# Optimization experiments

Measured on AMD Instinct MI355X. Metric: run time of the kernel, lower is better.

## Reference

```python
import jax, jax.numpy as jnp
import numpy as np

B, IN, H = 16384, 10, 1024
GD_ITERS, GD_LR = 7, 0.001


def setup_inputs() -> dict:
    key = jax.random.key(0)
    ks = jax.random.split(key, 16)
    s_in = 1.0 / np.sqrt(IN)
    s_h = 1.0 / np.sqrt(H)
    inp = {
        'x': jax.random.normal(ks[0], (B, IN), jnp.float32),
        'hidden': jax.random.normal(ks[1], (B, H), jnp.float32),
        'c': jax.random.normal(ks[2], (B, H), jnp.float32),
        'mid_price': jax.random.normal(ks[3], (B,), jnp.float32),
        # nn.Linear weights are [out, in]; biases [out]
        'Wf_w': jax.random.uniform(ks[4], (H, IN), jnp.float32, -s_in, s_in),
        'Wf_b': jax.random.uniform(ks[5], (H,), jnp.float32, -s_in, s_in),
        'Uf_w': jax.random.uniform(ks[6], (H, H), jnp.float32, -s_h, s_h),
        'Wi_w': jax.random.uniform(ks[7], (H, IN), jnp.float32, -s_in, s_in),
        'Wi_b': jax.random.uniform(ks[8], (H,), jnp.float32, -s_in, s_in),
        'Ui_w': jax.random.uniform(ks[9], (H, H), jnp.float32, -s_h, s_h),
        'Wc_w': jax.random.uniform(ks[10], (H, IN), jnp.float32, -s_in, s_in),
        'Wc_b': jax.random.uniform(ks[11], (H,), jnp.float32, -s_in, s_in),
        'Uc_w': jax.random.uniform(ks[12], (H, H), jnp.float32, -s_h, s_h),
        'Wo_w': jax.random.uniform(ks[13], (H, IN), jnp.float32, -s_in, s_in),
        'Wo_b': jax.random.uniform(ks[14], (H,), jnp.float32, -s_in, s_in),
        'Uo_w': jax.random.uniform(ks[15], (H, H), jnp.float32, -s_h, s_h),
    }
    return inp


def reference(x, hidden, c, mid_price, Wf_w, Wf_b, Uf_w, Wi_w, Wi_b, Ui_w,
              Wc_w, Wc_b, Uc_w, Wo_w, Wo_b, Uo_w):
    mp = mid_price.reshape(-1, 1)                       # [B,1]
    f_t = jax.nn.sigmoid(x @ Wf_w.T + Wf_b + hidden @ Uf_w.T)
    i_t = jax.nn.sigmoid(x @ Wi_w.T + Wi_b + hidden @ Ui_w.T)
    c_tilda = jnp.tanh(x @ Wc_w.T + Wc_b + hidden @ Uc_w.T)
    o_t = jax.nn.sigmoid(x @ Wo_w.T + Wo_b + hidden @ Uo_w.T)
    c_new = f_t * c + i_t * c_tilda
    h_std = o_t * jnp.tanh(c_new)
    r_t = jnp.concatenate([f_t, i_t, c_tilda, o_t, c_new, h_std], axis=1)  # [B,6H]

    bsz = r_t.shape[0]
    theta = jnp.zeros((6 * H, 1), dtype=r_t.dtype)

    def gd_step(_, th):
        err = r_t @ th - mp                             # [B,1]
        grad = 2.0 * (r_t.T @ err) / bsz                # [6H,1]
        return th - GD_LR * grad

    theta = jax.lax.fori_loop(0, GD_ITERS, gd_step, theta)

    importance = jnp.mean(jnp.abs(theta.reshape(6, H)), axis=1)  # [6]
    max_idx = jnp.argmax(importance)
    h_new = jax.lax.dynamic_slice(r_t, (0, max_idx * H), (bsz, H))
    return (h_new, c_new)
```

## Files before the change

kernel.cpp:

```cpp
#include <hip/hip_runtime.h>
#include <cstdint>
#include <cstddef>

#define Bsz   16384
#define INsz  10
#define Hsz   1024
#define N4    4096
#define K2    1056
#define SIXH  6144
#define GDI   7
#define LR    0.001f
#define NPART 512

typedef _Float16 f16;
typedef __attribute__((ext_vector_type(8))) _Float16 f16x8;
typedef __attribute__((ext_vector_type(4))) _Float16 f16x4;
typedef __attribute__((ext_vector_type(4))) float    f32x4;

__device__ __forceinline__ void llds16(const f16* g, f16* l) {
    __builtin_amdgcn_global_load_lds(
        (__attribute__((address_space(1))) void*)(uintptr_t)g,
        (__attribute__((address_space(3))) void*)(uintptr_t)l,
        16, 0, 0);
}

__device__ __forceinline__ float sigm(float z)   { return 1.f / (1.f + __expf(-z)); }
__device__ __forceinline__ float tanh_f(float z) { return 1.f - 2.f / (__expf(2.f * z) + 1.f); }

__global__ void k_prepU(const float* __restrict__ Uf, const float* __restrict__ Ui,
                        const float* __restrict__ Uc, const float* __restrict__ Uo,
                        const float* __restrict__ Wf, const float* __restrict__ Wi,
                        const float* __restrict__ Wc, const float* __restrict__ Wo,
                        f16* __restrict__ U2) {
    int idx = blockIdx.x * 256 + threadIdx.x;
    int n = idx / K2;
    int j = idx - n * K2;
    int g = n >> 10, h = n & 1023;
    const float* U = (g == 0) ? Uf : (g == 1) ? Ui : (g == 2) ? Uc : Uo;
    const float* W = (g == 0) ? Wf : (g == 1) ? Wi : (g == 2) ? Wc : Wo;
    float v = 0.f;
    if (j < Hsz)              v = U[(size_t)h * Hsz + j];
    else if (j < Hsz + INsz)  v = W[h * INsz + (j - Hsz)];
    U2[idx] = (f16)v;
}

__global__ void k_zero(float* __restrict__ p, int n) {
    int i = blockIdx.x * 256 + threadIdx.x;
    if (i < n) p[i] = 0.f;
}

__global__ __launch_bounds__(256, 2) void k_gemm(const float* __restrict__ hid,
                                                 const float* __restrict__ x,
                                                 const f16* __restrict__ U2,
                                                 const float* __restrict__ bf_,
                                                 const float* __restrict__ bi_,
                                                 const float* __restrict__ bc_,
                                                 const float* __restrict__ bo_,
                                                 f16* __restrict__ rt4) {
    __shared__ __align__(16) f16 As[128 * 32];
    __shared__ __align__(16) f16 Bs[128 * 32];
    const int tid  = threadIdx.x;
    const int bn   = blockIdx.x & 31;
    const int bm   = blockIdx.x >> 5;
    const int wave = tid >> 6, lane = tid & 63;
    const int wr = wave >> 1, wc = wave & 1;
    const int r = lane & 15, q = lane >> 4;

    const int arow = tid >> 2, acol = (tid & 3) * 8;
    const float* ga = hid + (size_t)(bm * 128 + arow) * Hsz + acol;
    const f16*   gb = U2  + (size_t)(bn * 128 + arow) * K2 + acol;
    f16* lB = &Bs[tid * 8];

    f32x4 acc[4][4];
#pragma unroll
    for (int i = 0; i < 4; ++i)
#pragma unroll
        for (int j = 0; j < 4; ++j) acc[i][j] = (f32x4){0.f, 0.f, 0.f, 0.f};

    for (int kt = 0; kt < K2; kt += 32) {
        float a0[8], a1[8];
        if (kt < Hsz) {
            float4 t0 = *(const float4*)(ga + kt);
            float4 t1 = *(const float4*)(ga + kt + 4);
            float4 t2 = *(const float4*)(ga + kt + (size_t)64 * Hsz);
            float4 t3 = *(const float4*)(ga + kt + (size_t)64 * Hsz + 4);
            a0[0]=t0.x; a0[1]=t0.y; a0[2]=t0.z; a0[3]=t0.w;
            a0[4]=t1.x; a0[5]=t1.y; a0[6]=t1.z; a0[7]=t1.w;
            a1[0]=t2.x; a1[1]=t2.y; a1[2]=t2.z; a1[3]=t2.w;
            a1[4]=t3.x; a1[5]=t3.y; a1[6]=t3.z; a1[7]=t3.w;
        } else {
#pragma unroll
            for (int k = 0; k < 8; ++k) {
                int c = acol + k;
                a0[k] = (c < INsz) ? x[(size_t)(bm * 128 + arow) * INsz + c] : 0.f;
                a1[k] = (c < INsz) ? x[(size_t)(bm * 128 + arow + 64) * INsz + c] : 0.f;
            }
        }
        __syncthreads();
        llds16(gb + kt,                   lB);
        llds16(gb + kt + (size_t)64 * K2, lB + 2048);
        f16x8 h0, h1;
#pragma unroll
        for (int k = 0; k < 8; ++k) { h0[k] = (f16)a0[k]; h1[k] = (f16)a1[k]; }
        *(f16x8*)&As[tid * 8]        = h0;
        *(f16x8*)&As[tid * 8 + 2048] = h1;
        __syncthreads();

        f16x8 af[4], bf[4];
#pragma unroll
        for (int i = 0; i < 4; ++i)
            af[i] = *(const f16x8*)&As[(wr * 64 + i * 16 + r) * 32 + q * 8];
#pragma unroll
        for (int j = 0; j < 4; ++j)
            bf[j] = *(const f16x8*)&Bs[(wc * 64 + j * 16 + r) * 32 + q * 8];
#pragma unroll
        for (int i = 0; i < 4; ++i)
#pragma unroll
            for (int j = 0; j < 4; ++j)
                acc[i][j] = __builtin_amdgcn_mfma_f32_16x16x32_f16(af[i], bf[j], acc[i][j], 0, 0, 0);
    }

    const int g = bn >> 3;
    const int h_base = (bn & 7) * 128;
    const float* Bb = (g == 0) ? bf_ : (g == 1) ? bi_ : (g == 2) ? bc_ : bo_;
    float bias[4];
#pragma unroll
    for (int j = 0; j < 4; ++j) bias[j] = Bb[h_base + wc * 64 + j * 16 + r];
#pragma unroll
    for (int i = 0; i < 4; ++i)
#pragma unroll
        for (int j = 0; j < 4; ++j)
#pragma unroll
            for (int reg = 0; reg < 4; ++reg) {
                int row_l = wr * 64 + i * 16 + q * 4 + reg;
                int col_l = wc * 64 + j * 16 + r;
                rt4[(size_t)(bm * 128 + row_l) * N4 + bn * 128 + col_l]
                    = (f16)(acc[i][j][reg] + bias[j]);
            }
}

__global__ void k_epi(f16* __restrict__ rt4, const float* __restrict__ c,
                      float* __restrict__ c_out) {
    int idx = blockIdx.x * 256 + threadIdx.x;
    int b = idx >> 10, h = idx & 1023;
    size_t zb = (size_t)b * N4 + h;
    float f  = sigm((float)rt4[zb]);
    float i_ = sigm((float)rt4[zb + 1024]);
    float ct = tanh_f((float)rt4[zb + 2048]);
    float o  = sigm((float)rt4[zb + 3072]);
    float cn = f * c[idx] + i_ * ct;
    rt4[zb]        = (f16)f;
    rt4[zb + 1024] = (f16)i_;
    rt4[zb + 2048] = (f16)ct;
    rt4[zb + 3072] = (f16)o;
    c_out[idx] = cn;
}

__global__ __launch_bounds__(256) void k_gd(const f16* __restrict__ rt4,
                                            const float* __restrict__ cn,
                                            const float* __restrict__ mp,
                                            const float* __restrict__ theta,
                                            float* __restrict__ part) {
    const int tid = threadIdx.x;
    const int r0 = blockIdx.x * 32;
    const int wave = tid >> 6, lane = tid & 63;

    float thA[8], thB[8], thC[4], thD[4];
    float grA[8] = {0}, grB[8] = {0}, grC[4] = {0}, grD[4] = {0};
#pragma unroll
    for (int k = 0; k < 8; ++k) {
        thA[k] = theta[tid * 8 + k];
        thB[k] = theta[2048 + tid * 8 + k];
    }
#pragma unroll
    for (int k = 0; k < 4; ++k) {
        thC[k] = theta[4096 + tid * 4 + k];
        thD[k] = theta[5120 + tid * 4 + k];
    }

    __shared__ float red[16];

    for (int rb = 0; rb < 32; rb += 4) {
        f16x8 dA[4], dB[4];
        f32x4 dC[4];
        float hs[4][4];
        float s[4];
#pragma unroll
        for (int rr = 0; rr < 4; ++rr) {
            const size_t row = (size_t)(r0 + rb + rr);
            dA[rr] = *(const f16x8*)&rt4[row * N4 + tid * 8];
            dB[rr] = *(const f16x8*)&rt4[row * N4 + 2048 + tid * 8];
            dC[rr] = *(const f32x4*)&cn[row * Hsz + tid * 4];
            f16x4 dO = *(const f16x4*)&rt4[row * N4 + 3072 + tid * 4];
            float a = 0.f;
#pragma unroll
            for (int k = 0; k < 8; ++k) a += (float)dA[rr][k] * thA[k];
#pragma unroll
            for (int k = 0; k < 8; ++k) a += (float)dB[rr][k] * thB[k];
#pragma unroll
            for (int k = 0; k < 4; ++k) {
                float h = (float)dO[k] * tanh_f(dC[rr][k]);
                hs[rr][k] = h;
                a += dC[rr][k] * thC[k] + h * thD[k];
            }
            s[rr] = a;
        }
#pragma unroll
        for (int rr = 0; rr < 4; ++rr)
#pragma unroll
            for (int off = 32; off > 0; off >>= 1)
                s[rr] += __shfl_xor(s[rr], off, 64);
        if (lane == 0) {
#pragma unroll
            for (int rr = 0; rr < 4; ++rr) red[rr * 4 + wave] = s[rr];
        }
        __syncthreads();
        float e[4];
#pragma unroll
        for (int rr = 0; rr < 4; ++rr)
            e[rr] = (red[rr * 4 + 0] + red[rr * 4 + 1] + red[rr * 4 + 2] + red[rr * 4 + 3])
                    - mp[r0 + rb + rr];
        __syncthreads();
#pragma unroll
        for (int rr = 0; rr < 4; ++rr) {
#pragma unroll
            for (int k = 0; k < 8; ++k) {
                grA[k] += e[rr] * (float)dA[rr][k];
                grB[k] += e[rr] * (float)dB[rr][k];
            }
#pragma unroll
            for (int k = 0; k < 4; ++k) {
                grC[k] += e[rr] * dC[rr][k];
                grD[k] += e[rr] * hs[rr][k];
            }
        }
    }

    float* pb = &part[(size_t)blockIdx.x * SIXH];
#pragma unroll
    for (int k = 0; k < 8; ++k) {
        pb[tid * 8 + k]        = grA[k];
        pb[2048 + tid * 8 + k] = grB[k];
    }
#pragma unroll
    for (int k = 0; k < 4; ++k) {
        pb[4096 + tid * 4 + k] = grC[k];
        pb[5120 + tid * 4 + k] = grD[k];
    }
}

__global__ void k_reduce(const float* __restrict__ part, float* __restrict__ theta) {
    __shared__ float sred[256];
    const int tid = threadIdx.x;
    const int c = (tid & 31) + blockIdx.x * 32;
    const int pl = tid >> 5;
    float s = 0.f;
    for (int p = pl; p < NPART; p += 8) s += part[(size_t)p * SIXH + c];
    sred[tid] = s;
    __syncthreads();
    if (pl == 0) {
        float acc = s;
#pragma unroll
        for (int k = 1; k < 8; ++k) acc += sred[k * 32 + (tid & 31)];
        theta[c] -= (2.f * LR / (float)Bsz) * acc;
    }
}

__global__ void k_argmax(const float* __restrict__ theta, float* __restrict__ outc) {
    __shared__ float w[6][4];
    const int tid = threadIdx.x;
    const int wave = tid >> 6, lane = tid & 63;
    for (int g = 0; g < 6; ++g) {
        float s = 0.f;
        for (int j = tid; j < 1024; j += 256) s += fabsf(theta[g * 1024 + j]);
#pragma unroll
        for (int off = 32; off > 0; off >>= 1) s += __shfl_xor(s, off, 64);
        if (lane == 0) w[g][wave] = s;
    }
    __syncthreads();
    if (tid == 0) {
        int best = 0;
        float bv = w[0][0] + w[0][1] + w[0][2] + w[0][3];
        for (int g = 1; g < 6; ++g) {
            float v = w[g][0] + w[g][1] + w[g][2] + w[g][3];
            if (v > bv) { bv = v; best = g; }
        }
        outc[0] = (float)best;
    }
}

__global__ void k_gather(const f16* __restrict__ rt4, const float* __restrict__ cnp,
                         float* __restrict__ outh) {
    const int idx = (int)cnp[0];
    int t = blockIdx.x * 256 + threadIdx.x;
    int b = t >> 8, h4 = (t & 255) * 4;
    float* o = &outh[(size_t)b * Hsz + h4];
    if (idx < 4) {
        f16x4 v = *(const f16x4*)&rt4[(size_t)b * N4 + idx * 1024 + h4];
#pragma unroll
        for (int k = 0; k < 4; ++k) o[k] = (float)v[k];
    } else if (idx == 4) {
        f32x4 v = *(const f32x4*)&cnp[(size_t)b * Hsz + h4];
#pragma unroll
        for (int k = 0; k < 4; ++k) o[k] = v[k];
    } else {
        f16x4 ov = *(const f16x4*)&rt4[(size_t)b * N4 + 3072 + h4];
        f32x4 cv = *(const f32x4*)&cnp[(size_t)b * Hsz + h4];
#pragma unroll
        for (int k = 0; k < 4; ++k) o[k] = (float)ov[k] * tanh_f(cv[k]);
    }
}

__global__ void k_fix(const f16* __restrict__ rt4, const float* __restrict__ c_in,
                      float* __restrict__ out) {
    if (threadIdx.x == 0 && blockIdx.x == 0) {
        int idx = (int)out[(size_t)Bsz * Hsz];
        float f  = (float)rt4[0];
        float i_ = (float)rt4[1024];
        float ct = (float)rt4[2048];
        float o  = (float)rt4[3072];
        float cn = f * c_in[0] + i_ * ct;
        out[(size_t)Bsz * Hsz] = cn;
        if (idx == 4)      out[0] = cn;
        else if (idx == 5) out[0] = o * tanh_f(cn);
    }
}

extern "C" void kernel_launch(void* const* d_in, const int* in_sizes, int n_in,
                              void* d_out, int out_size, void* d_ws, size_t ws_size,
                              hipStream_t stream) {
    const float* x    = (const float*)d_in[0];
    const float* hid  = (const float*)d_in[1];
    const float* c    = (const float*)d_in[2];
    const float* mp   = (const float*)d_in[3];
    const float* Wf_w = (const float*)d_in[4];
    const float* Wf_b = (const float*)d_in[5];
    const float* Uf_w = (const float*)d_in[6];
    const float* Wi_w = (const float*)d_in[7];
    const float* Wi_b = (const float*)d_in[8];
    const float* Ui_w = (const float*)d_in[9];
    const float* Wc_w = (const float*)d_in[10];
    const float* Wc_b = (const float*)d_in[11];
    const float* Uc_w = (const float*)d_in[12];
    const float* Wo_w = (const float*)d_in[13];
    const float* Wo_b = (const float*)d_in[14];
    const float* Uo_w = (const float*)d_in[15];
    float* out  = (float*)d_out;
    float* outc = out + (size_t)Bsz * Hsz;

    f16* rt4 = (f16*)d_ws;
    uint8_t* oh = (uint8_t*)d_out;
    f16*   U2    = (f16*)oh;
    float* theta = (float*)(oh + 8650752);
    float* part  = (float*)(oh + 8675328);

    k_prepU<<<(N4 * K2) / 256, 256, 0, stream>>>(Uf_w, Ui_w, Uc_w, Uo_w,
                                                 Wf_w, Wi_w, Wc_w, Wo_w, U2);
    k_gemm<<<4096, 256, 0, stream>>>(hid, x, U2, Wf_b, Wi_b, Wc_b, Wo_b, rt4);
    k_epi<<<(Bsz * Hsz) / 256, 256, 0, stream>>>(rt4, c, outc);
    k_zero<<<24, 256, 0, stream>>>(theta, SIXH);
    for (int it = 0; it < GDI; ++it) {
        k_gd<<<NPART, 256, 0, stream>>>(rt4, outc, mp, theta, part);
        k_reduce<<<SIXH / 32, 256, 0, stream>>>(part, theta);
    }
    k_argmax<<<1, 256, 0, stream>>>(theta, outc);
    k_gather<<<(Bsz * Hsz / 4) / 256, 256, 0, stream>>>(rt4, outc, out);
    k_fix<<<1, 64, 0, stream>>>(rt4, c, out);
}
```

Baseline: 927.4 us.

## Pre-pack A/B into MFMA tile order, pipeline GEMM, fuse gate epilogue

Adds a prep kernel that converts hidden and x into fp16 in MFMA fragment-tiled order, with a ones column so the bias folds into the packed weights. The GEMM now streams both operands straight to LDS through a triple-buffered global_load_lds pipeline, remaps block IDs for locality, and runs at higher occupancy. Columns are permuted so each block holds all four gates for 32 hidden units, which lets the sigmoid/tanh and c_new epilogue run in-kernel through a swizzled LDS image and removes the separate epilogue pass over rt4. The cost is an extra pass that writes packed A to a scratch region inside the output buffer.

```diff
diff --git a/kernel.cpp b/kernel.cpp
--- a/kernel.cpp
+++ b/kernel.cpp
@@ -6,7 +6,7 @@
 #define INsz  10
 #define Hsz   1024
 #define N4    4096
-#define K2    1056
+#define NK    34
 #define SIXH  6144
 #define GDI   7
 #define LR    0.001f
@@ -27,21 +27,73 @@
 __device__ __forceinline__ float sigm(float z)   { return 1.f / (1.f + __expf(-z)); }
 __device__ __forceinline__ float tanh_f(float z) { return 1.f - 2.f / (__expf(2.f * z) + 1.f); }
 
+
+__global__ void k_prepA(const float* __restrict__ hid, const float* __restrict__ x,
+                        f16* __restrict__ A2) {
+    int c = blockIdx.x * 256 + threadIdx.x;
+    int mt  = c / 17408;
+    int rem = c - mt * 17408;
+    int ks  = rem >> 9;
+    int rb  = (rem >> 6) & 7;
+    int l   = rem & 63;
+    int row = mt * 128 + rb * 16 + (l & 15);
+    int k0  = ks * 32 + (l >> 4) * 8;
+    f16x8 v;
+    if (k0 + 8 <= Hsz) {
+        float4 t0 = *(const float4*)&hid[(size_t)row * Hsz + k0];
+        float4 t1 = *(const float4*)&hid[(size_t)row * Hsz + k0 + 4];
+        v[0]=(f16)t0.x; v[1]=(f16)t0.y; v[2]=(f16)t0.z; v[3]=(f16)t0.w;
+        v[4]=(f16)t1.x; v[5]=(f16)t1.y; v[6]=(f16)t1.z; v[7]=(f16)t1.w;
+    } else {
+#pragma unroll
+        for (int e = 0; e < 8; ++e) {
+            int k = k0 + e;
+            float f = 0.f;
+            if (k < Hsz + INsz)       f = x[(size_t)row * INsz + (k - Hsz)];
+            else if (k == Hsz + INsz) f = 1.0f;
+            v[e] = (f16)f;
+        }
+    }
+    *(f16x8*)&A2[(size_t)c * 8] = v;
+}
+
 __global__ void k_prepU(const float* __restrict__ Uf, const float* __restrict__ Ui,
                         const float* __restrict__ Uc, const float* __restrict__ Uo,
                         const float* __restrict__ Wf, const float* __restrict__ Wi,
                         const float* __restrict__ Wc, const float* __restrict__ Wo,
+                        const float* __restrict__ bf_, const float* __restrict__ bi_,
+                        const float* __restrict__ bc_, const float* __restrict__ bo_,
                         f16* __restrict__ U2) {
-    int idx = blockIdx.x * 256 + threadIdx.x;
-    int n = idx / K2;
-    int j = idx - n * K2;
-    int g = n >> 10, h = n & 1023;
+    int c = blockIdx.x * 256 + threadIdx.x;
+    int nt  = c / 17408;
+    int rem = c - nt * 17408;
+    int ks  = rem >> 9;
+    int rb  = (rem >> 6) & 7;
+    int l   = rem & 63;
+    int cc  = rb * 16 + (l & 15);
+    int g   = cc >> 5;
+    int h   = nt * 32 + (cc & 31);
+    int k0  = ks * 32 + (l >> 4) * 8;
     const float* U = (g == 0) ? Uf : (g == 1) ? Ui : (g == 2) ? Uc : Uo;
-    const float* W = (g == 0) ? Wf : (g == 1) ? Wi : (g == 2) ? Wc : Wo;
-    float v = 0.f;
-    if (j < Hsz)              v = U[(size_t)h * Hsz + j];
-    else if (j < Hsz + INsz)  v = W[h * INsz + (j - Hsz)];
-    U2[idx] = (f16)v;
+    f16x8 v;
+    if (k0 + 8 <= Hsz) {
+        float4 t0 = *(const float4*)&U[(size_t)h * Hsz + k0];
+        float4 t1 = *(const float4*)&U[(size_t)h * Hsz + k0 + 4];
+        v[0]=(f16)t0.x; v[1]=(f16)t0.y; v[2]=(f16)t0.z; v[3]=(f16)t0.w;
+        v[4]=(f16)t1.x; v[5]=(f16)t1.y; v[6]=(f16)t1.z; v[7]=(f16)t1.w;
+    } else {
+        const float* W  = (g == 0) ? Wf  : (g == 1) ? Wi  : (g == 2) ? Wc  : Wo;
+        const float* Bb = (g == 0) ? bf_ : (g == 1) ? bi_ : (g == 2) ? bc_ : bo_;
+#pragma unroll
+        for (int e = 0; e < 8; ++e) {
+            int k = k0 + e;
+            float f = 0.f;
+            if (k < Hsz + INsz)       f = W[h * INsz + (k - Hsz)];
+            else if (k == Hsz + INsz) f = Bb[h];
+            v[e] = (f16)f;
+        }
+    }
+    *(f16x8*)&U2[(size_t)c * 8] = v;
 }
 
 __global__ void k_zero(float* __restrict__ p, int n) {
@@ -49,27 +101,33 @@
     if (i < n) p[i] = 0.f;
 }
 
-__global__ __launch_bounds__(256, 2) void k_gemm(const float* __restrict__ hid,
-                                                 const float* __restrict__ x,
+#define IMG(r, cidx) ((r) * 128 + ((cidx) ^ (((r) & 15) << 3)))
+
+__global__ __launch_bounds__(256, 3) void k_gemm(const f16* __restrict__ A2,
                                                  const f16* __restrict__ U2,
-                                                 const float* __restrict__ bf_,
-                                                 const float* __restrict__ bi_,
-                                                 const float* __restrict__ bc_,
-                                                 const float* __restrict__ bo_,
-                                                 f16* __restrict__ rt4) {
-    __shared__ __align__(16) f16 As[128 * 32];
-    __shared__ __align__(16) f16 Bs[128 * 32];
-    const int tid  = threadIdx.x;
-    const int bn   = blockIdx.x & 31;
-    const int bm   = blockIdx.x >> 5;
-    const int wave = tid >> 6, lane = tid & 63;
+                                                 const float* __restrict__ c_in,
+                                                 f16* __restrict__ rt4,
+                                                 float* __restrict__ c_out) {
+    __shared__ __align__(16) f16 sm[3 * 8192];
+    const int bid = blockIdx.x;
+    const int swz = ((bid & 7) << 9) | (bid >> 3);
+    const int bm = swz >> 5, bn = swz & 31;
+    const int tid = threadIdx.x, wave = tid >> 6, lane = tid & 63;
     const int wr = wave >> 1, wc = wave & 1;
     const int r = lane & 15, q = lane >> 4;
 
-    const int arow = tid >> 2, acol = (tid & 3) * 8;
-    const float* ga = hid + (size_t)(bm * 128 + arow) * Hsz + acol;
-    const f16*   gb = U2  + (size_t)(bn * 128 + arow) * K2 + acol;
-    f16* lB = &Bs[tid * 8];
+    const f16* gA = A2 + (size_t)bm * (NK * 4096);
+    const f16* gB = U2 + (size_t)bn * (NK * 4096);
+
+    auto stage = [&](int ks) {
+        f16* s = &sm[(ks % 3) * 8192];
+        const f16* a = gA + (size_t)ks * 4096;
+        const f16* b = gB + (size_t)ks * 4096;
+        llds16(a + tid * 8,        &s[tid * 8]);
+        llds16(a + 2048 + tid * 8, &s[2048 + tid * 8]);
+        llds16(b + tid * 8,        &s[4096 + tid * 8]);
+        llds16(b + 2048 + tid * 8, &s[6144 + tid * 8]);
+    };
 
     f32x4 acc[4][4];
 #pragma unroll
@@ -77,42 +135,30 @@
 #pragma unroll
         for (int j = 0; j < 4; ++j) acc[i][j] = (f32x4){0.f, 0.f, 0.f, 0.f};
 
-    for (int kt = 0; kt < K2; kt += 32) {
-        float a0[8], a1[8];
-        if (kt < Hsz) {
-            float4 t0 = *(const float4*)(ga + kt);
-            float4 t1 = *(const float4*)(ga + kt + 4);
-            float4 t2 = *(const float4*)(ga + kt + (size_t)64 * Hsz);
-            float4 t3 = *(const float4*)(ga + kt + (size_t)64 * Hsz + 4);
-            a0[0]=t0.x; a0[1]=t0.y; a0[2]=t0.z; a0[3]=t0.w;
-            a0[4]=t1.x; a0[5]=t1.y; a0[6]=t1.z; a0[7]=t1.w;
-            a1[0]=t2.x; a1[1]=t2.y; a1[2]=t2.z; a1[3]=t2.w;
-            a1[4]=t3.x; a1[5]=t3.y; a1[6]=t3.z; a1[7]=t3.w;
+    stage(0); stage(1);
+
+    for (int ks = 0; ks < NK; ++ks) {
+        if (ks + 2 < NK) {
+            stage(ks + 2);
+            asm volatile("s_waitcnt vmcnt(8)" ::: "memory");
+        } else if (ks + 1 < NK) {
+            asm volatile("s_waitcnt vmcnt(4)" ::: "memory");
         } else {
-#pragma unroll
-            for (int k = 0; k < 8; ++k) {
-                int c = acol + k;
-                a0[k] = (c < INsz) ? x[(size_t)(bm * 128 + arow) * INsz + c] : 0.f;
-                a1[k] = (c < INsz) ? x[(size_t)(bm * 128 + arow + 64) * INsz + c] : 0.f;
-            }
-        }
-        __syncthreads();
-        llds16(gb + kt,                   lB);
-        llds16(gb + kt + (size_t)64 * K2, lB + 2048);
-        f16x8 h0, h1;
-#pragma unroll
-        for (int k = 0; k < 8; ++k) { h0[k] = (f16)a0[k]; h1[k] = (f16)a1[k]; }
-        *(f16x8*)&As[tid * 8]        = h0;
-        *(f16x8*)&As[tid * 8 + 2048] = h1;
-        __syncthreads();
-
+            asm volatile("s_waitcnt vmcnt(0)" ::: "memory");
+        }
+        __builtin_amdgcn_s_barrier();
+        __builtin_amdgcn_sched_barrier(0);
+        const f16* s = &sm[(ks % 3) * 8192];
         f16x8 af[4], bf[4];
 #pragma unroll
         for (int i = 0; i < 4; ++i)
-            af[i] = *(const f16x8*)&As[(wr * 64 + i * 16 + r) * 32 + q * 8];
+            af[i] = *(const f16x8*)&s[(wr * 4 + i) * 512 + lane * 8];
 #pragma unroll
         for (int j = 0; j < 4; ++j)
-            bf[j] = *(const f16x8*)&Bs[(wc * 64 + j * 16 + r) * 32 + q * 8];
+            bf[j] = *(const f16x8*)&s[4096 + (wc * 4 + j) * 512 + lane * 8];
+        asm volatile("s_waitcnt lgkmcnt(0)" ::: "memory");
+        __builtin_amdgcn_sched_barrier(0);
+        __builtin_amdgcn_s_barrier();
 #pragma unroll
         for (int i = 0; i < 4; ++i)
 #pragma unroll
@@ -120,12 +166,7 @@
                 acc[i][j] = __builtin_amdgcn_mfma_f32_16x16x32_f16(af[i], bf[j], acc[i][j], 0, 0, 0);
     }
 
-    const int g = bn >> 3;
-    const int h_base = (bn & 7) * 128;
-    const float* Bb = (g == 0) ? bf_ : (g == 1) ? bi_ : (g == 2) ? bc_ : bo_;
-    float bias[4];
-#pragma unroll
-    for (int j = 0; j < 4; ++j) bias[j] = Bb[h_base + wc * 64 + j * 16 + r];
+    f16* img = sm;
 #pragma unroll
     for (int i = 0; i < 4; ++i)
 #pragma unroll
@@ -134,26 +175,44 @@
             for (int reg = 0; reg < 4; ++reg) {
                 int row_l = wr * 64 + i * 16 + q * 4 + reg;
                 int col_l = wc * 64 + j * 16 + r;
-                rt4[(size_t)(bm * 128 + row_l) * N4 + bn * 128 + col_l]
-                    = (f16)(acc[i][j][reg] + bias[j]);
+                img[IMG(row_l, col_l)] = (f16)acc[i][j][reg];
             }
-}
-
-__global__ void k_epi(f16* __restrict__ rt4, const float* __restrict__ c,
-                      float* __restrict__ c_out) {
-    int idx = blockIdx.x * 256 + threadIdx.x;
-    int b = idx >> 10, h = idx & 1023;
-    size_t zb = (size_t)b * N4 + h;
-    float f  = sigm((float)rt4[zb]);
-    float i_ = sigm((float)rt4[zb + 1024]);
-    float ct = tanh_f((float)rt4[zb + 2048]);
-    float o  = sigm((float)rt4[zb + 3072]);
-    float cn = f * c[idx] + i_ * ct;
-    rt4[zb]        = (f16)f;
-    rt4[zb + 1024] = (f16)i_;
-    rt4[zb + 2048] = (f16)ct;
-    rt4[zb + 3072] = (f16)o;
-    c_out[idx] = cn;
+    asm volatile("s_waitcnt lgkmcnt(0)" ::: "memory");
+    __builtin_amdgcn_s_barrier();
+    __builtin_amdgcn_sched_barrier(0);
+
+    const int bcol = bn * 32;
+#pragma unroll
+    for (int s_ = 0; s_ < 2; ++s_) {
+        int a  = s_ * 256 + tid;
+        int row = a >> 2, ho = (a & 3) * 8;
+        int grow = bm * 128 + row;
+        f16x8 pf = *(const f16x8*)&img[IMG(row,      ho)];
+        f16x8 pi = *(const f16x8*)&img[IMG(row, 32 + ho)];
+        f16x8 pc = *(const f16x8*)&img[IMG(row, 64 + ho)];
+        f16x8 po = *(const f16x8*)&img[IMG(row, 96 + ho)];
+        float4 c0 = *(const float4*)&c_in[(size_t)grow * Hsz + bcol + ho];
+        float4 c1 = *(const float4*)&c_in[(size_t)grow * Hsz + bcol + ho + 4];
+        float cv[8] = {c0.x, c0.y, c0.z, c0.w, c1.x, c1.y, c1.z, c1.w};
+        f16x8 of, oi, oc, oo;
+        float cn[8];
+#pragma unroll
+        for (int e = 0; e < 8; ++e) {
+            float f  = sigm((float)pf[e]);
+            float i_ = sigm((float)pi[e]);
+            float ct = tanh_f((float)pc[e]);
+            float o  = sigm((float)po[e]);
+            cn[e] = f * cv[e] + i_ * ct;
+            of[e] = (f16)f; oi[e] = (f16)i_; oc[e] = (f16)ct; oo[e] = (f16)o;
+        }
+        size_t rb_ = (size_t)grow * N4 + bcol + ho;
+        *(f16x8*)&rt4[rb_]        = of;
+        *(f16x8*)&rt4[rb_ + 1024] = oi;
+        *(f16x8*)&rt4[rb_ + 2048] = oc;
+        *(f16x8*)&rt4[rb_ + 3072] = oo;
+        *(float4*)&c_out[(size_t)grow * Hsz + bcol + ho]     = (float4){cn[0], cn[1], cn[2], cn[3]};
+        *(float4*)&c_out[(size_t)grow * Hsz + bcol + ho + 4] = (float4){cn[4], cn[5], cn[6], cn[7]};
+    }
 }
 
 __global__ __launch_bounds__(256) void k_gd(const f16* __restrict__ rt4,
@@ -351,13 +410,15 @@
     f16* rt4 = (f16*)d_ws;
     uint8_t* oh = (uint8_t*)d_out;
     f16*   U2    = (f16*)oh;
-    float* theta = (float*)(oh + 8650752);
-    float* part  = (float*)(oh + 8675328);
-
-    k_prepU<<<(N4 * K2) / 256, 256, 0, stream>>>(Uf_w, Ui_w, Uc_w, Uo_w,
-                                                 Wf_w, Wi_w, Wc_w, Wo_w, U2);
-    k_gemm<<<4096, 256, 0, stream>>>(hid, x, U2, Wf_b, Wi_b, Wc_b, Wo_b, rt4);
-    k_epi<<<(Bsz * Hsz) / 256, 256, 0, stream>>>(rt4, c, outc);
+    f16*   A2    = (f16*)(oh + 8912896);
+    float* theta = (float*)(oh + 44564480);
+    float* part  = (float*)(oh + 44589056);
+
+    k_prepU<<<2176, 256, 0, stream>>>(Uf_w, Ui_w, Uc_w, Uo_w,
+                                      Wf_w, Wi_w, Wc_w, Wo_w,
+                                      Wf_b, Wi_b, Wc_b, Wo_b, U2);
+    k_prepA<<<8704, 256, 0, stream>>>(hid, x, A2);
+    k_gemm<<<4096, 256, 0, stream>>>(A2, U2, c, rt4, outc);
     k_zero<<<24, 256, 0, stream>>>(theta, SIXH);
     for (int it = 0; it < GDI; ++it) {
         k_gd<<<NPART, 256, 0, stream>>>(rt4, outc, mp, theta, part);
```

New measurement: 866.9 us. 1.07x faster.
